# Performance work log

Hardware: AMD Instinct MI355X
Metric: run time of the kernel (lower is better)

## Reference

```python
import jax, jax.numpy as jnp
import numpy as np

N_NODES = 50000
N_EDGES = 800000
C = 128


def setup_inputs() -> dict:
    key = jax.random.key(0)
    ks = jax.random.split(key, 7)
    X_real = jax.random.normal(ks[0], (N_NODES, C), dtype=jnp.float32)
    X_imag = jax.random.normal(ks[1], (N_NODES, C), dtype=jnp.float32)
    # sparse normalized Laplacian values (real/imag parts), COO format
    L_real_vals = jax.random.normal(ks[2], (N_EDGES,), dtype=jnp.float32) * 0.1
    L_imag_vals = jax.random.normal(ks[3], (N_EDGES,), dtype=jnp.float32) * 0.1
    weight = jax.random.normal(ks[4], (C, C), dtype=jnp.float32) * (1.0 / np.sqrt(C))
    row = jax.random.randint(ks[5], (N_EDGES,), 0, N_NODES, dtype=jnp.int32)
    col = jax.random.randint(ks[6], (N_EDGES,), 0, N_NODES, dtype=jnp.int32)
    return {"X_real": X_real, "X_imag": X_imag,
            "L_real_vals": L_real_vals, "L_imag_vals": L_imag_vals,
            "weight": weight, "row": row, "col": col}


def reference(X_real, X_imag, L_real_vals, L_imag_vals, weight, row, col):
    n = X_real.shape[0]

    def spmm(vals, X):
        # sparse [N,N] @ dense [N,C] via gather + segment-sum scatter
        return jax.ops.segment_sum(vals[:, None] * X[col], row, num_segments=n)

    # complex Laplacian application: (Lr + i Li)(Xr + i Xi)
    # real = Lr@Xr - Li@Xi ; imag = Li@Xr + Lr@Xi ; then shared dense projection W
    agg_real = spmm(L_real_vals, X_real) - spmm(L_imag_vals, X_imag)  # [N, C]
    agg_imag = spmm(L_imag_vals, X_real) + spmm(L_real_vals, X_imag)  # [N, C]
    result_real = agg_real @ weight
    result_imag = agg_imag @ weight
    # residual add as in forward()
    return (result_real + X_real, result_imag + X_imag)
```

## Files before the change

kernel.cpp:

```cpp
#include <hip/hip_runtime.h>
#include <cstddef>

#define CC 128

typedef __attribute__((ext_vector_type(8))) short bf16x8;
typedef __attribute__((ext_vector_type(4))) float f32x4;


__device__ __forceinline__ unsigned short f2bf(float f)
{
    unsigned int u = __float_as_uint(f);
    u = (u + 0x7fffu + ((u >> 16) & 1u)) >> 16;
    return (unsigned short)u;
}

__device__ __forceinline__ unsigned int pack2(float a, float b)
{
    return (unsigned int)f2bf(a) | ((unsigned int)f2bf(b) << 16);
}

__global__ __launch_bounds__(256) void hist_conv_fused(
    const int* __restrict__ row, int* __restrict__ counts,
    int* __restrict__ rank, int N, int E,
    const float* __restrict__ W, unsigned short* __restrict__ Wt, int G_conv)
{
    const int bid = blockIdx.x;
    if (bid < G_conv) {
        const int idx = bid * 256 + threadIdx.x;
        if (idx >= CC * CC) return;
        const int k = idx >> 7;
        const int n = idx & 127;
        const unsigned int sw =
            ((unsigned)(2 * k) ^ (((unsigned)n & 7u) << 4)) >> 1;
        Wt[(size_t)n * 128 + sw] = f2bf(W[idx]);
        return;
    }
    const int base = ((bid - G_conv) * 256 + threadIdx.x) * 4;
    if (base + 3 < E) {
        const int4 r4 = *(const int4*)(row + base);
        int4 k4;
        k4.x = atomicAdd(counts + 0 * N + r4.x, 1);
        k4.y = atomicAdd(counts + 1 * N + r4.y, 1);
        k4.z = atomicAdd(counts + 2 * N + r4.z, 1);
        k4.w = atomicAdd(counts + 3 * N + r4.w, 1);
        *(int4*)(rank + base) = k4;
    } else {
        for (int e = base; e < E; ++e)
            rank[e] = atomicAdd(counts + (size_t)(e & 3) * N + row[e], 1);
    }
}

__global__ __launch_bounds__(256) void scan_block_reduce(
    const int* __restrict__ counts, int* __restrict__ bsum, int N)
{
    __shared__ int s[256];
    const int t = threadIdx.x;
    const int idx = blockIdx.x * 256 + t;
    int v = 0;
    if (idx < N)
        v = counts[idx] + counts[N + idx] + counts[2 * N + idx]
          + counts[3 * N + idx];
    s[t] = v;
    __syncthreads();
    #pragma unroll
    for (int off = 128; off > 0; off >>= 1) {
        if (t < off) s[t] += s[t + off];
        __syncthreads();
    }
    if (t == 0) bsum[blockIdx.x] = s[0];
}

__global__ __launch_bounds__(256) void scan_bsum(
    const int* __restrict__ bsum, int* __restrict__ bpre, int NB)
{
    __shared__ int s[256];
    const int t = threadIdx.x;
    s[t] = (t < NB) ? bsum[t] : 0;
    __syncthreads();
    #pragma unroll
    for (int off = 1; off < 256; off <<= 1) {
        const int v = s[t];
        const int u = (t >= off) ? s[t - off] : 0;
        __syncthreads();
        s[t] = v + u;
        __syncthreads();
    }
    if (t < NB) bpre[t] = t ? s[t - 1] : 0;
}

__global__ __launch_bounds__(256) void scan_final(
    const int* __restrict__ counts, const int* __restrict__ bpre,
    int* __restrict__ rbase, int N)
{
    __shared__ int s[256];
    const int t = threadIdx.x;
    const int idx = blockIdx.x * 256 + t;
    int c0 = 0, c1 = 0, c2 = 0, c3 = 0;
    if (idx < N) {
        c0 = counts[idx];
        c1 = counts[N + idx];
        c2 = counts[2 * N + idx];
        c3 = counts[3 * N + idx];
    }
    const int v = c0 + c1 + c2 + c3;
    s[t] = v;
    __syncthreads();
    #pragma unroll
    for (int off = 1; off < 256; off <<= 1) {
        const int a = s[t];
        const int u = (t >= off) ? s[t - off] : 0;
        __syncthreads();
        s[t] = a + u;
        __syncthreads();
    }
    if (idx < N) {
        const int off = bpre[blockIdx.x] + s[t] - v;
        rbase[idx]         = off;
        rbase[N + idx]     = off + c0;
        rbase[2 * N + idx] = off + c0 + c1;
        rbase[3 * N + idx] = off + c0 + c1 + c2;
    }
}

__device__ __forceinline__ void gemm_body(
    const float* __restrict__ Xr, const float* __restrict__ Xi,
    const unsigned short* __restrict__ Wt,
    unsigned short* __restrict__ Y, int N, int bid)
{
    __shared__ unsigned short Bs[128 * 128];
    __shared__ unsigned short As[64 * 128];
    const int t = threadIdx.x;
    const int m0 = bid * 64;
    const int M = 2 * N;

    {
        const uint4* src = (const uint4*)Wt;
        uint4* dst = (uint4*)Bs;
        #pragma unroll
        for (int i = 0; i < 8; ++i) dst[t + 256 * i] = src[t + 256 * i];
    }
    #pragma unroll
    for (int i = 0; i < 4; ++i) {
        const int blk = t + 256 * i;
        const int r  = blk >> 4;
        const int k0 = (blk & 15) * 8;
        const int m  = m0 + r;
        float4 q0 = make_float4(0.f, 0.f, 0.f, 0.f);
        float4 q1 = make_float4(0.f, 0.f, 0.f, 0.f);
        if (m < M) {
            const float* src = (m < N) ? (Xr + (size_t)m * CC)
                                       : (Xi + (size_t)(m - N) * CC);
            q0 = *(const float4*)(src + k0);
            q1 = *(const float4*)(src + k0 + 4);
        }
        uint4 h;
        h.x = pack2(q0.x, q0.y);
        h.y = pack2(q0.z, q0.w);
        h.z = pack2(q1.x, q1.y);
        h.w = pack2(q1.z, q1.w);
        const int byte = r * 256 + ((2 * k0) ^ ((r & 7) << 4));
        *(uint4*)((char*)As + byte) = h;
    }
    __syncthreads();

    const int w = t >> 6, lane = t & 63;
    const int wr = w >> 1, wc = w & 1;
    const int r0 = wr * 32;
    const int c0 = wc * 64;
    const int lr = lane & 15;
    const int lk = lane >> 4;

    f32x4 acc[2][4];
    #pragma unroll
    for (int a = 0; a < 2; ++a)
        #pragma unroll
        for (int b = 0; b < 4; ++b)
            acc[a][b] = (f32x4){0.f, 0.f, 0.f, 0.f};

    #pragma unroll
    for (int kk = 0; kk < 4; ++kk) {
        const int kbase = kk * 32 + lk * 8;
        bf16x8 afrag[2];
        #pragma unroll
        for (int at = 0; at < 2; ++at) {
            const int row = r0 + at * 16 + lr;
            afrag[at] = *(const bf16x8*)((const char*)As +
                row * 256 + ((2 * kbase) ^ ((row & 7) << 4)));
        }
        #pragma unroll
        for (int bt = 0; bt < 4; ++bt) {
            const int col = c0 + bt * 16 + lr;
            const bf16x8 bfrag = *(const bf16x8*)((const char*)Bs +
                col * 256 + ((2 * kbase) ^ ((col & 7) << 4)));
            acc[0][bt] = __builtin_amdgcn_mfma_f32_16x16x32_bf16(
                afrag[0], bfrag, acc[0][bt], 0, 0, 0);
            acc[1][bt] = __builtin_amdgcn_mfma_f32_16x16x32_bf16(
                afrag[1], bfrag, acc[1][bt], 0, 0, 0);
        }
    }

    #pragma unroll
    for (int at = 0; at < 2; ++at) {
        #pragma unroll
        for (int v = 0; v < 4; ++v) {
            const int m = m0 + r0 + at * 16 + lk * 4 + v;
            if (m >= M) continue;
            const int node = (m < N) ? m : m - N;
            const int half = (m < N) ? 0 : 128;
            unsigned short* dst = Y + (size_t)node * 256 + half;
            #pragma unroll
            for (int bt = 0; bt < 4; ++bt)
                dst[c0 + bt * 16 + lr] = f2bf(acc[at][bt][v]);
        }
    }
}

__device__ __forceinline__ void fill_body(
    const int* __restrict__ row, const int* __restrict__ col,
    const float* __restrict__ Lr, const float* __restrict__ Li,
    const int* __restrict__ rbase, const int* __restrict__ rank,
    int4* __restrict__ meta, int N, int E, int bid)
{
    const int base = (bid * 256 + threadIdx.x) * 4;
    if (base + 3 < E) {
        const int4   r4 = *(const int4*)(row + base);
        const int4   c4 = *(const int4*)(col + base);
        const float4 a4 = *(const float4*)(Lr + base);
        const float4 b4 = *(const float4*)(Li + base);
        const int4   k4 = *(const int4*)(rank + base);
        meta[rbase[r4.x] + k4.x] =
            make_int4(c4.x, __float_as_int(a4.x), __float_as_int(b4.x), 0);
        meta[rbase[N + r4.y] + k4.y] =
            make_int4(c4.y, __float_as_int(a4.y), __float_as_int(b4.y), 0);
        meta[rbase[2 * N + r4.z] + k4.z] =
            make_int4(c4.z, __float_as_int(a4.z), __float_as_int(b4.z), 0);
        meta[rbase[3 * N + r4.w] + k4.w] =
            make_int4(c4.w, __float_as_int(a4.w), __float_as_int(b4.w), 0);
    } else {
        for (int e = base; e < E; ++e)
            meta[rbase[(size_t)(e & 3) * N + row[e]] + rank[e]] =
                make_int4(col[e], __float_as_int(Lr[e]), __float_as_int(Li[e]), 0);
    }
}

__global__ __launch_bounds__(256) void fill_gemm_fused(
    const int* __restrict__ row, const int* __restrict__ col,
    const float* __restrict__ Lr, const float* __restrict__ Li,
    const int* __restrict__ rbase, const int* __restrict__ rank,
    int4* __restrict__ meta,
    const float* __restrict__ Xr, const float* __restrict__ Xi,
    const unsigned short* __restrict__ Wt, unsigned short* __restrict__ Y,
    int N, int E, int G_gemm)
{
    const int bid = blockIdx.x;
    if (bid < G_gemm)
        gemm_body(Xr, Xi, Wt, Y, N, bid);
    else
        fill_body(row, col, Lr, Li, rbase, rank, meta, N, E, bid - G_gemm);
}

__device__ __forceinline__ void cmadd_bf(
    const int4 m, const unsigned int ur, const unsigned int ui,
    float2& aR, float2& aI)
{
    const float lr = __int_as_float(m.y);
    const float li = __int_as_float(m.z);
    const float yrx = __uint_as_float(ur << 16);
    const float yry = __uint_as_float(ur & 0xFFFF0000u);
    const float yix = __uint_as_float(ui << 16);
    const float yiy = __uint_as_float(ui & 0xFFFF0000u);
    aR.x += lr * yrx - li * yix;
    aR.y += lr * yry - li * yiy;
    aI.x += li * yrx + lr * yix;
    aI.y += li * yry + lr * yiy;
}

__device__ __forceinline__ void edge_acc(
    const int4 m, const unsigned short* __restrict__ Y,
    int lane, float2& aR, float2& aI)
{
    const unsigned short* b = Y + (size_t)m.x * 256 + 2 * lane;
    const unsigned int ur = *(const unsigned int*)(b);
    const unsigned int ui = *(const unsigned int*)(b + 128);
    cmadd_bf(m, ur, ui, aR, aI);
}

__global__ __launch_bounds__(256) void gather_fused(
    const unsigned short* __restrict__ Y,
    const float* __restrict__ Xr, const float* __restrict__ Xi,
    const int* __restrict__ offsets, const int4* __restrict__ meta,
    float* __restrict__ out, int N, int E)
{
    const int n = blockIdx.x * 4 + (threadIdx.x >> 6);
    if (n >= N) return;
    const int lane = threadIdx.x & 63;
    const int start = offsets[n];
    const int end   = (n + 1 < N) ? offsets[n + 1] : E;
    const int Em1 = E - 1;

    float2 aR = *(const float2*)(Xr + (size_t)n * CC + 2 * lane);
    float2 aI = *(const float2*)(Xi + (size_t)n * CC + 2 * lane);

    int4 m0 = meta[min(start + 0, Em1)];
    int4 m1 = meta[min(start + 1, Em1)];
    int4 m2 = meta[min(start + 2, Em1)];
    int4 m3 = meta[min(start + 3, Em1)];
    int4 m4 = meta[min(start + 4, Em1)];
    int4 m5 = meta[min(start + 5, Em1)];
    int4 m6 = meta[min(start + 6, Em1)];
    int4 m7 = meta[min(start + 7, Em1)];

    int j = start;
    for (; j + 8 <= end; j += 8) {
        const int4 n0 = meta[min(j +  8, Em1)];
        const int4 n1 = meta[min(j +  9, Em1)];
        const int4 n2 = meta[min(j + 10, Em1)];
        const int4 n3 = meta[min(j + 11, Em1)];
        const int4 n4 = meta[min(j + 12, Em1)];
        const int4 n5 = meta[min(j + 13, Em1)];
        const int4 n6 = meta[min(j + 14, Em1)];
        const int4 n7 = meta[min(j + 15, Em1)];
        const unsigned short* b0 = Y + (size_t)m0.x * 256 + 2 * lane;
        const unsigned short* b1 = Y + (size_t)m1.x * 256 + 2 * lane;
        const unsigned short* b2 = Y + (size_t)m2.x * 256 + 2 * lane;
        const unsigned short* b3 = Y + (size_t)m3.x * 256 + 2 * lane;
        const unsigned short* b4 = Y + (size_t)m4.x * 256 + 2 * lane;
        const unsigned short* b5 = Y + (size_t)m5.x * 256 + 2 * lane;
        const unsigned short* b6 = Y + (size_t)m6.x * 256 + 2 * lane;
        const unsigned short* b7 = Y + (size_t)m7.x * 256 + 2 * lane;
        const unsigned int ur0 = *(const unsigned int*)(b0);
        const unsigned int ui0 = *(const unsigned int*)(b0 + 128);
        const unsigned int ur1 = *(const unsigned int*)(b1);
        const unsigned int ui1 = *(const unsigned int*)(b1 + 128);
        const unsigned int ur2 = *(const unsigned int*)(b2);
        const unsigned int ui2 = *(const unsigned int*)(b2 + 128);
        const unsigned int ur3 = *(const unsigned int*)(b3);
        const unsigned int ui3 = *(const unsigned int*)(b3 + 128);
        const unsigned int ur4 = *(const unsigned int*)(b4);
        const unsigned int ui4 = *(const unsigned int*)(b4 + 128);
        const unsigned int ur5 = *(const unsigned int*)(b5);
        const unsigned int ui5 = *(const unsigned int*)(b5 + 128);
        const unsigned int ur6 = *(const unsigned int*)(b6);
        const unsigned int ui6 = *(const unsigned int*)(b6 + 128);
        const unsigned int ur7 = *(const unsigned int*)(b7);
        const unsigned int ui7 = *(const unsigned int*)(b7 + 128);

        cmadd_bf(m0, ur0, ui0, aR, aI);
        cmadd_bf(m1, ur1, ui1, aR, aI);
        cmadd_bf(m2, ur2, ui2, aR, aI);
        cmadd_bf(m3, ur3, ui3, aR, aI);
        cmadd_bf(m4, ur4, ui4, aR, aI);
        cmadd_bf(m5, ur5, ui5, aR, aI);
        cmadd_bf(m6, ur6, ui6, aR, aI);
        cmadd_bf(m7, ur7, ui7, aR, aI);

        m0 = n0; m1 = n1; m2 = n2; m3 = n3;
        m4 = n4; m5 = n5; m6 = n6; m7 = n7;
    }
    const int r = end - j;
    if (r > 0) edge_acc(m0, Y, lane, aR, aI);
    if (r > 1) edge_acc(m1, Y, lane, aR, aI);
    if (r > 2) edge_acc(m2, Y, lane, aR, aI);
    if (r > 3) edge_acc(m3, Y, lane, aR, aI);
    if (r > 4) edge_acc(m4, Y, lane, aR, aI);
    if (r > 5) edge_acc(m5, Y, lane, aR, aI);
    if (r > 6) edge_acc(m6, Y, lane, aR, aI);

    *(float2*)(out + (size_t)n * CC + 2 * lane) = aR;
    *(float2*)(out + ((size_t)n + N) * CC + 2 * lane) = aI;
}

__global__ __launch_bounds__(256) void gather_nodes(
    const float* __restrict__ Xr, const float* __restrict__ Xi,
    const int* __restrict__ offsets, const int4* __restrict__ meta,
    float* __restrict__ out, int N, int E)
{
    const int n = blockIdx.x * 4 + (threadIdx.x >> 6);
    if (n >= N) return;
    const int lane = threadIdx.x & 63;
    const int start = offsets[n];
    const int end   = (n + 1 < N) ? offsets[n + 1] : E;
    float2 aR = make_float2(0.f, 0.f);
    float2 aI = make_float2(0.f, 0.f);
    for (int j = start; j < end; ++j) {
        const int4 m0 = meta[j];
        const float2 xr0 = *(const float2*)(Xr + (size_t)m0.x * CC + 2 * lane);
        const float2 xi0 = *(const float2*)(Xi + (size_t)m0.x * CC + 2 * lane);
        const float lr0 = __int_as_float(m0.y), li0 = __int_as_float(m0.z);
        aR.x += lr0 * xr0.x - li0 * xi0.x;
        aR.y += lr0 * xr0.y - li0 * xi0.y;
        aI.x += li0 * xr0.x + lr0 * xi0.x;
        aI.y += li0 * xr0.y + lr0 * xi0.y;
    }
    *(float2*)(out + (size_t)n * CC + 2 * lane) = aR;
    *(float2*)(out + ((size_t)n + N) * CC + 2 * lane) = aI;
}

__global__ __launch_bounds__(256) void scatter_edges(
    const float* __restrict__ Xr, const float* __restrict__ Xi,
    const float* __restrict__ Lr, const float* __restrict__ Li,
    const int* __restrict__ row, const int* __restrict__ col,
    float* __restrict__ out, int N, int E)
{
    const int e = blockIdx.x * 4 + (threadIdx.x >> 6);
    if (e >= E) return;
    const int lane = threadIdx.x & 63;
    const int r = row[e], c = col[e];
    const float lr = Lr[e];
    const float li = Li[e];
    const float2 xr = *(const float2*)(Xr + (size_t)c * CC + 2 * lane);
    const float2 xi = *(const float2*)(Xi + (size_t)c * CC + 2 * lane);
    float* pr = out + (size_t)r * CC + 2 * lane;
    float* pi = out + ((size_t)r + N) * CC + 2 * lane;
    unsafeAtomicAdd(pr,     lr * xr.x - li * xi.x);
    unsafeAtomicAdd(pr + 1, lr * xr.y - li * xi.y);
    unsafeAtomicAdd(pi,     li * xr.x + lr * xi.x);
    unsafeAtomicAdd(pi + 1, li * xr.y + lr * xi.y);
}

__global__ __launch_bounds__(256) void hist_rank_fb(
    const int* __restrict__ row, int* __restrict__ counts,
    int* __restrict__ rank, int N, int E)
{
    const int base = (blockIdx.x * 256 + threadIdx.x) * 4;
    if (base + 3 < E) {
        const int4 r4 = *(const int4*)(row + base);
        int4 k4;
        k4.x = atomicAdd(counts + 0 * N + r4.x, 1);
        k4.y = atomicAdd(counts + 1 * N + r4.y, 1);
        k4.z = atomicAdd(counts + 2 * N + r4.z, 1);
        k4.w = atomicAdd(counts + 3 * N + r4.w, 1);
        *(int4*)(rank + base) = k4;
    } else {
        for (int e = base; e < E; ++e)
            rank[e] = atomicAdd(counts + (size_t)(e & 3) * N + row[e], 1);
    }
}

__global__ __launch_bounds__(256) void fill_csr_fb(
    const int* __restrict__ row, const int* __restrict__ col,
    const float* __restrict__ Lr, const float* __restrict__ Li,
    const int* __restrict__ rbase, const int* __restrict__ rank,
    int4* __restrict__ meta, int N, int E)
{
    fill_body(row, col, Lr, Li, rbase, rank, meta, N, E, blockIdx.x);
}

__global__ __launch_bounds__(256) void gemm_inplace(
    float* __restrict__ io, const float* __restrict__ W,
    const float* __restrict__ Xp, int N)
{
    __shared__ float Ws[64 * CC];
    __shared__ float AsT[CC][36];
    const int t = threadIdx.x;
    const int m0 = blockIdx.x * 32;

    for (int ch = t; ch < 1024; ch += 256) {
        const int r  = ch >> 5;
        const int k0 = (ch & 31) * 4;
        const int m  = m0 + r;
        float4 q = make_float4(0.f, 0.f, 0.f, 0.f);
        if (m < N) q = *(const float4*)(io + (size_t)m * CC + k0);
        AsT[k0 + 0][r] = q.x;
        AsT[k0 + 1][r] = q.y;
        AsT[k0 + 2][r] = q.z;
        AsT[k0 + 3][r] = q.w;
    }

    const int cg = t & 31;
    const int rs = t >> 5;
    float s[4][4];
    #pragma unroll
    for (int a = 0; a < 4; ++a)
        #pragma unroll
        for (int b = 0; b < 4; ++b) s[a][b] = 0.f;

    for (int kc = 0; kc < 2; ++kc) {
        __syncthreads();
        {
            const float4* src = (const float4*)(W + (size_t)kc * 64 * CC);
            float4* dst = (float4*)Ws;
            #pragma unroll
            for (int i = 0; i < 8; ++i) dst[t + 256 * i] = src[t + 256 * i];
        }
        __syncthreads();
        #pragma unroll 4
        for (int kk = 0; kk < 64; ++kk) {
            const int k = kc * 64 + kk;
            const float4 av = *(const float4*)&AsT[k][rs * 4];
            const float4 wv = *(const float4*)&Ws[kk * CC + cg * 4];
            const float ar[4] = {av.x, av.y, av.z, av.w};
            const float wc[4] = {wv.x, wv.y, wv.z, wv.w};
            #pragma unroll
            for (int a = 0; a < 4; ++a)
                #pragma unroll
                for (int b = 0; b < 4; ++b) s[a][b] += ar[a] * wc[b];
        }
    }

    #pragma unroll
    for (int a = 0; a < 4; ++a) {
        const int m = m0 + rs * 4 + a;
        if (m >= N) continue;
        const float4 xv = *(const float4*)(Xp + (size_t)m * CC + cg * 4);
        float4 o;
        o.x = s[a][0] + xv.x;
        o.y = s[a][1] + xv.y;
        o.z = s[a][2] + xv.z;
        o.w = s[a][3] + xv.w;
        *(float4*)(io + (size_t)m * CC + cg * 4) = o;
    }
}

extern "C" void kernel_launch(void* const* d_in, const int* in_sizes, int n_in,
                              void* d_out, int out_size, void* d_ws, size_t ws_size,
                              hipStream_t stream)
{
    const float* Xr = (const float*)d_in[0];
    const float* Xi = (const float*)d_in[1];
    const float* Lr = (const float*)d_in[2];
    const float* Li = (const float*)d_in[3];
    const float* W  = (const float*)d_in[4];
    const int* row = (const int*)d_in[5];
    const int* col = (const int*)d_in[6];
    float* out = (float*)d_out;

    const int N = in_sizes[0] / CC;
    const int E = in_sizes[2];
    const int NB = (N + 255) / 256;
    const int EB4 = ((E + 3) / 4 + 255) / 256;
    const int G_conv = (CC * CC + 255) / 256;
    const int G_gemm = (2 * N + 63) / 64;

    const size_t y_bytes    = (size_t)N * 256 * sizeof(unsigned short);
    const size_t wt_bytes   = (size_t)CC * CC * sizeof(unsigned short);
    const size_t meta_bytes = (size_t)E * 16;
    const size_t int_bytes  = ((size_t)8 * N + 512 + E) * sizeof(int);
    const size_t need_csr   = meta_bytes + int_bytes;
    const size_t need_fused = y_bytes + wt_bytes + need_csr;

    if (ws_size >= need_fused) {
        unsigned short* Y  = (unsigned short*)d_ws;
        unsigned short* Wt = (unsigned short*)((char*)d_ws + y_bytes);
        int4*  meta   = (int4*)((char*)d_ws + y_bytes + wt_bytes);
        int*   counts = (int*)((char*)d_ws + y_bytes + wt_bytes + meta_bytes);
        int*   rbase  = counts + 4 * N;
        int*   bsum   = rbase + 4 * N;
        int*   bpre   = bsum + 256;
        int*   rank   = bpre + 256;

        hipMemsetAsync(counts, 0, (size_t)4 * N * sizeof(int), stream);
        hist_conv_fused<<<dim3(G_conv + EB4), dim3(256), 0, stream>>>(
            row, counts, rank, N, E, W, Wt, G_conv);
        scan_block_reduce<<<dim3(NB), dim3(256), 0, stream>>>(counts, bsum, N);
        scan_bsum<<<dim3(1), dim3(256), 0, stream>>>(bsum, bpre, NB);
        scan_final<<<dim3(NB), dim3(256), 0, stream>>>(counts, bpre, rbase, N);
        fill_gemm_fused<<<dim3(G_gemm + EB4), dim3(256), 0, stream>>>(
            row, col, Lr, Li, rbase, rank, meta, Xr, Xi, Wt, Y, N, E, G_gemm);
        gather_fused<<<dim3((N + 3) / 4), dim3(256), 0, stream>>>(
            Y, Xr, Xi, rbase , meta, out, N, E);
    } else if (ws_size >= need_csr) {
        int4* meta    = (int4*)d_ws;
        int*  counts  = (int*)((char*)d_ws + meta_bytes);
        int*  rbase   = counts + 4 * N;
        int*  bsum    = rbase + 4 * N;
        int*  bpre    = bsum + 256;
        int*  rank    = bpre + 256;

        hipMemsetAsync(counts, 0, (size_t)4 * N * sizeof(int), stream);
        hist_rank_fb<<<dim3(EB4), dim3(256), 0, stream>>>(row, counts, rank, N, E);
        scan_block_reduce<<<dim3(NB), dim3(256), 0, stream>>>(counts, bsum, N);
        scan_bsum<<<dim3(1), dim3(256), 0, stream>>>(bsum, bpre, NB);
        scan_final<<<dim3(NB), dim3(256), 0, stream>>>(counts, bpre, rbase, N);
        fill_csr_fb<<<dim3(EB4), dim3(256), 0, stream>>>(
            row, col, Lr, Li, rbase, rank, meta, N, E);
        gather_nodes<<<dim3((N + 3) / 4), dim3(256), 0, stream>>>(
            Xr, Xi, rbase, meta, out, N, E);
        gemm_inplace<<<dim3((N + 31) / 32), dim3(256), 0, stream>>>(out, W, Xr, N);
        gemm_inplace<<<dim3((N + 31) / 32), dim3(256), 0, stream>>>(
            out + (size_t)N * CC, W, Xi, N);
    } else {
        hipMemsetAsync(out, 0, (size_t)2 * N * CC * sizeof(float), stream);
        scatter_edges<<<dim3((E + 3) / 4), dim3(256), 0, stream>>>(
            Xr, Xi, Lr, Li, row, col, out, N, E);
        gemm_inplace<<<dim3((N + 31) / 32), dim3(256), 0, stream>>>(out, W, Xr, N);
        gemm_inplace<<<dim3((N + 31) / 32), dim3(256), 0, stream>>>(
            out + (size_t)N * CC, W, Xi, N);
    }
}
```

Measured before the change: 247.0 us.

## Fuse whole pipeline into one persistent cooperative kernel with grid syncs

Replaces the memset plus six separate launches (histogram, three scan stages, fill+GEMM, gather) with a single cooperative persistent kernel that loops over work and separates phases with grid-wide syncs. It also reorders work so the GEMM tile runs alongside the histogram phase, and loads the weight tile into LDS once per block instead of once per tile. The aim is to remove launch gaps and tail effects between many small kernels. The trade-offs are the cost of grid syncs, a grid capped at occupancy-limited residency (48KB LDS per block), and persistent loops that may underuse the GPU in the gather phase. If the cooperative launch fails, it falls back to the old multi-kernel path.

```diff
diff --git a/kernel.cpp b/kernel.cpp
--- a/kernel.cpp
+++ b/kernel.cpp
@@ -1,11 +1,13 @@
 #include <hip/hip_runtime.h>
+#include <hip/hip_cooperative_groups.h>
 #include <cstddef>
 
 #define CC 128
+
+namespace cg = cooperative_groups;
 
 typedef __attribute__((ext_vector_type(8))) short bf16x8;
 typedef __attribute__((ext_vector_type(4))) float f32x4;
-
 
 __device__ __forceinline__ unsigned short f2bf(float f)
 {
@@ -19,126 +21,24 @@
     return (unsigned int)f2bf(a) | ((unsigned int)f2bf(b) << 16);
 }
 
-__global__ __launch_bounds__(256) void hist_conv_fused(
-    const int* __restrict__ row, int* __restrict__ counts,
-    int* __restrict__ rank, int N, int E,
-    const float* __restrict__ W, unsigned short* __restrict__ Wt, int G_conv)
-{
-    const int bid = blockIdx.x;
-    if (bid < G_conv) {
-        const int idx = bid * 256 + threadIdx.x;
-        if (idx >= CC * CC) return;
-        const int k = idx >> 7;
-        const int n = idx & 127;
-        const unsigned int sw =
-            ((unsigned)(2 * k) ^ (((unsigned)n & 7u) << 4)) >> 1;
-        Wt[(size_t)n * 128 + sw] = f2bf(W[idx]);
-        return;
-    }
-    const int base = ((bid - G_conv) * 256 + threadIdx.x) * 4;
-    if (base + 3 < E) {
-        const int4 r4 = *(const int4*)(row + base);
-        int4 k4;
-        k4.x = atomicAdd(counts + 0 * N + r4.x, 1);
-        k4.y = atomicAdd(counts + 1 * N + r4.y, 1);
-        k4.z = atomicAdd(counts + 2 * N + r4.z, 1);
-        k4.w = atomicAdd(counts + 3 * N + r4.w, 1);
-        *(int4*)(rank + base) = k4;
-    } else {
-        for (int e = base; e < E; ++e)
-            rank[e] = atomicAdd(counts + (size_t)(e & 3) * N + row[e], 1);
-    }
-}
-
-__global__ __launch_bounds__(256) void scan_block_reduce(
-    const int* __restrict__ counts, int* __restrict__ bsum, int N)
-{
-    __shared__ int s[256];
-    const int t = threadIdx.x;
-    const int idx = blockIdx.x * 256 + t;
-    int v = 0;
-    if (idx < N)
-        v = counts[idx] + counts[N + idx] + counts[2 * N + idx]
-          + counts[3 * N + idx];
-    s[t] = v;
-    __syncthreads();
-    #pragma unroll
-    for (int off = 128; off > 0; off >>= 1) {
-        if (t < off) s[t] += s[t + off];
-        __syncthreads();
-    }
-    if (t == 0) bsum[blockIdx.x] = s[0];
-}
-
-__global__ __launch_bounds__(256) void scan_bsum(
-    const int* __restrict__ bsum, int* __restrict__ bpre, int NB)
-{
-    __shared__ int s[256];
-    const int t = threadIdx.x;
-    s[t] = (t < NB) ? bsum[t] : 0;
-    __syncthreads();
-    #pragma unroll
-    for (int off = 1; off < 256; off <<= 1) {
-        const int v = s[t];
-        const int u = (t >= off) ? s[t - off] : 0;
-        __syncthreads();
-        s[t] = v + u;
-        __syncthreads();
-    }
-    if (t < NB) bpre[t] = t ? s[t - 1] : 0;
-}
-
-__global__ __launch_bounds__(256) void scan_final(
-    const int* __restrict__ counts, const int* __restrict__ bpre,
-    int* __restrict__ rbase, int N)
-{
-    __shared__ int s[256];
-    const int t = threadIdx.x;
-    const int idx = blockIdx.x * 256 + t;
-    int c0 = 0, c1 = 0, c2 = 0, c3 = 0;
-    if (idx < N) {
-        c0 = counts[idx];
-        c1 = counts[N + idx];
-        c2 = counts[2 * N + idx];
-        c3 = counts[3 * N + idx];
-    }
-    const int v = c0 + c1 + c2 + c3;
-    s[t] = v;
-    __syncthreads();
-    #pragma unroll
-    for (int off = 1; off < 256; off <<= 1) {
-        const int a = s[t];
-        const int u = (t >= off) ? s[t - off] : 0;
-        __syncthreads();
-        s[t] = a + u;
-        __syncthreads();
-    }
-    if (idx < N) {
-        const int off = bpre[blockIdx.x] + s[t] - v;
-        rbase[idx]         = off;
-        rbase[N + idx]     = off + c0;
-        rbase[2 * N + idx] = off + c0 + c1;
-        rbase[3 * N + idx] = off + c0 + c1 + c2;
-    }
-}
-
-__device__ __forceinline__ void gemm_body(
+
+__device__ __forceinline__ void gemm_stage_B(
+    const unsigned short* __restrict__ Wt, unsigned short* Bs, int t)
+{
+    const uint4* src = (const uint4*)Wt;
+    uint4* dst = (uint4*)Bs;
+    #pragma unroll
+    for (int i = 0; i < 8; ++i) dst[t + 256 * i] = src[t + 256 * i];
+}
+
+__device__ __forceinline__ void gemm_tile(
     const float* __restrict__ Xr, const float* __restrict__ Xi,
-    const unsigned short* __restrict__ Wt,
-    unsigned short* __restrict__ Y, int N, int bid)
-{
-    __shared__ unsigned short Bs[128 * 128];
-    __shared__ unsigned short As[64 * 128];
-    const int t = threadIdx.x;
+    unsigned short* __restrict__ Y, int N, int bid,
+    const unsigned short* Bs, unsigned short* As, int t)
+{
     const int m0 = bid * 64;
     const int M = 2 * N;
 
-    {
-        const uint4* src = (const uint4*)Wt;
-        uint4* dst = (uint4*)Bs;
-        #pragma unroll
-        for (int i = 0; i < 8; ++i) dst[t + 256 * i] = src[t + 256 * i];
-    }
     #pragma unroll
     for (int i = 0; i < 4; ++i) {
         const int blk = t + 256 * i;
@@ -215,13 +115,12 @@
     }
 }
 
-__device__ __forceinline__ void fill_body(
+__device__ __forceinline__ void fill_quad(
     const int* __restrict__ row, const int* __restrict__ col,
     const float* __restrict__ Lr, const float* __restrict__ Li,
     const int* __restrict__ rbase, const int* __restrict__ rank,
-    int4* __restrict__ meta, int N, int E, int bid)
-{
-    const int base = (bid * 256 + threadIdx.x) * 4;
+    int4* __restrict__ meta, int N, int E, int base)
+{
     if (base + 3 < E) {
         const int4   r4 = *(const int4*)(row + base);
         const int4   c4 = *(const int4*)(col + base);
@@ -243,20 +142,22 @@
     }
 }
 
-__global__ __launch_bounds__(256) void fill_gemm_fused(
-    const int* __restrict__ row, const int* __restrict__ col,
-    const float* __restrict__ Lr, const float* __restrict__ Li,
-    const int* __restrict__ rbase, const int* __restrict__ rank,
-    int4* __restrict__ meta,
-    const float* __restrict__ Xr, const float* __restrict__ Xi,
-    const unsigned short* __restrict__ Wt, unsigned short* __restrict__ Y,
-    int N, int E, int G_gemm)
-{
-    const int bid = blockIdx.x;
-    if (bid < G_gemm)
-        gemm_body(Xr, Xi, Wt, Y, N, bid);
-    else
-        fill_body(row, col, Lr, Li, rbase, rank, meta, N, E, bid - G_gemm);
+__device__ __forceinline__ void hist_quad(
+    const int* __restrict__ row, int* __restrict__ counts,
+    int* __restrict__ rank, int N, int E, int base)
+{
+    if (base + 3 < E) {
+        const int4 r4 = *(const int4*)(row + base);
+        int4 k4;
+        k4.x = atomicAdd(counts + 0 * N + r4.x, 1);
+        k4.y = atomicAdd(counts + 1 * N + r4.y, 1);
+        k4.z = atomicAdd(counts + 2 * N + r4.z, 1);
+        k4.w = atomicAdd(counts + 3 * N + r4.w, 1);
+        *(int4*)(rank + base) = k4;
+    } else {
+        for (int e = base; e < E; ++e)
+            rank[e] = atomicAdd(counts + (size_t)(e & 3) * N + row[e], 1);
+    }
 }
 
 __device__ __forceinline__ void cmadd_bf(
@@ -285,15 +186,12 @@
     cmadd_bf(m, ur, ui, aR, aI);
 }
 
-__global__ __launch_bounds__(256) void gather_fused(
+__device__ __forceinline__ void gather_node(
     const unsigned short* __restrict__ Y,
     const float* __restrict__ Xr, const float* __restrict__ Xi,
     const int* __restrict__ offsets, const int4* __restrict__ meta,
-    float* __restrict__ out, int N, int E)
-{
-    const int n = blockIdx.x * 4 + (threadIdx.x >> 6);
-    if (n >= N) return;
-    const int lane = threadIdx.x & 63;
+    float* __restrict__ out, int N, int E, int n, int lane)
+{
     const int start = offsets[n];
     const int end   = (n + 1 < N) ? offsets[n + 1] : E;
     const int Em1 = E - 1;
@@ -370,6 +268,254 @@
     *(float2*)(out + ((size_t)n + N) * CC + 2 * lane) = aI;
 }
 
+__global__ __launch_bounds__(256) void mega(
+    const int* __restrict__ row, const int* __restrict__ col,
+    const float* __restrict__ Lr, const float* __restrict__ Li,
+    const float* __restrict__ W,
+    const float* __restrict__ Xr, const float* __restrict__ Xi,
+    int* __restrict__ counts, int* __restrict__ rank,
+    int* __restrict__ rbase, int* __restrict__ bsum, int* __restrict__ bpre,
+    int4* __restrict__ meta, unsigned short* __restrict__ Wt,
+    unsigned short* __restrict__ Y, float* __restrict__ out,
+    int N, int E, int NB, int G_gemm)
+{
+    cg::grid_group gg = cg::this_grid();
+    __shared__ char smem[49152];
+    unsigned short* Bs = (unsigned short*)smem;
+    unsigned short* As = (unsigned short*)(smem + 32768);
+    int* si = (int*)smem;
+
+    const int t  = threadIdx.x;
+    const int gb = blockIdx.x;
+    const int G  = gridDim.x;
+    const int NQ = (E + 3) >> 2;
+
+    for (int i = gb * 256 + t; i < 4 * N; i += G * 256) counts[i] = 0;
+    for (int idx = gb * 256 + t; idx < CC * CC; idx += G * 256) {
+        const int k = idx >> 7;
+        const int n = idx & 127;
+        const unsigned int sw =
+            ((unsigned)(2 * k) ^ (((unsigned)n & 7u) << 4)) >> 1;
+        Wt[(size_t)n * 128 + sw] = f2bf(W[idx]);
+    }
+    gg.sync();
+
+    gemm_stage_B(Wt, Bs, t);
+    for (int bid = gb; bid < G_gemm; bid += G) {
+        __syncthreads();
+        gemm_tile(Xr, Xi, Y, N, bid, Bs, As, t);
+    }
+    for (int qi = gb * 256 + t; qi < NQ; qi += G * 256)
+        hist_quad(row, counts, rank, N, E, qi * 4);
+    gg.sync();
+
+    for (int b = gb; b < NB; b += G) {
+        const int idx = b * 256 + t;
+        int v = 0;
+        if (idx < N)
+            v = counts[idx] + counts[N + idx] + counts[2 * N + idx]
+              + counts[3 * N + idx];
+        si[t] = v;
+        __syncthreads();
+        #pragma unroll
+        for (int off = 128; off > 0; off >>= 1) {
+            if (t < off) si[t] += si[t + off];
+            __syncthreads();
+        }
+        if (t == 0) bsum[b] = si[0];
+        __syncthreads();
+    }
+    gg.sync();
+
+    if (gb == 0) {
+        si[t] = (t < NB) ? bsum[t] : 0;
+        __syncthreads();
+        #pragma unroll
+        for (int off = 1; off < 256; off <<= 1) {
+            const int v = si[t];
+            const int u = (t >= off) ? si[t - off] : 0;
+            __syncthreads();
+            si[t] = v + u;
+            __syncthreads();
+        }
+        if (t < NB) bpre[t] = t ? si[t - 1] : 0;
+    }
+    gg.sync();
+
+    for (int b = gb; b < NB; b += G) {
+        const int idx = b * 256 + t;
+        int c0 = 0, c1 = 0, c2 = 0, c3 = 0;
+        if (idx < N) {
+            c0 = counts[idx];
+            c1 = counts[N + idx];
+            c2 = counts[2 * N + idx];
+            c3 = counts[3 * N + idx];
+        }
+        const int v = c0 + c1 + c2 + c3;
+        si[t] = v;
+        __syncthreads();
+        #pragma unroll
+        for (int off = 1; off < 256; off <<= 1) {
+            const int a = si[t];
+            const int u = (t >= off) ? si[t - off] : 0;
+            __syncthreads();
+            si[t] = a + u;
+            __syncthreads();
+        }
+        if (idx < N) {
+            const int off = bpre[b] + si[t] - v;
+            rbase[idx]         = off;
+            rbase[N + idx]     = off + c0;
+            rbase[2 * N + idx] = off + c0 + c1;
+            rbase[3 * N + idx] = off + c0 + c1 + c2;
+        }
+        __syncthreads();
+    }
+    gg.sync();
+
+    for (int qi = gb * 256 + t; qi < NQ; qi += G * 256)
+        fill_quad(row, col, Lr, Li, rbase, rank, meta, N, E, qi * 4);
+    gg.sync();
+
+    {
+        const int lane = t & 63;
+        const int wv = t >> 6;
+        const int NG = (N + 3) / 4;
+        for (int g = gb; g < NG; g += G) {
+            const int n = g * 4 + wv;
+            if (n < N)
+                gather_node(Y, Xr, Xi, rbase , meta, out, N, E,
+                            n, lane);
+        }
+    }
+}
+
+
+__global__ __launch_bounds__(256) void hist_conv_fused(
+    const int* __restrict__ row, int* __restrict__ counts,
+    int* __restrict__ rank, int N, int E,
+    const float* __restrict__ W, unsigned short* __restrict__ Wt, int G_conv)
+{
+    const int bid = blockIdx.x;
+    if (bid < G_conv) {
+        const int idx = bid * 256 + threadIdx.x;
+        if (idx >= CC * CC) return;
+        const int k = idx >> 7;
+        const int n = idx & 127;
+        const unsigned int sw =
+            ((unsigned)(2 * k) ^ (((unsigned)n & 7u) << 4)) >> 1;
+        Wt[(size_t)n * 128 + sw] = f2bf(W[idx]);
+        return;
+    }
+    hist_quad(row, counts, rank, N, E,
+              ((bid - G_conv) * 256 + threadIdx.x) * 4);
+}
+
+__global__ __launch_bounds__(256) void scan_block_reduce(
+    const int* __restrict__ counts, int* __restrict__ bsum, int N)
+{
+    __shared__ int s[256];
+    const int t = threadIdx.x;
+    const int idx = blockIdx.x * 256 + t;
+    int v = 0;
+    if (idx < N)
+        v = counts[idx] + counts[N + idx] + counts[2 * N + idx]
+          + counts[3 * N + idx];
+    s[t] = v;
+    __syncthreads();
+    #pragma unroll
+    for (int off = 128; off > 0; off >>= 1) {
+        if (t < off) s[t] += s[t + off];
+        __syncthreads();
+    }
+    if (t == 0) bsum[blockIdx.x] = s[0];
+}
+
+__global__ __launch_bounds__(256) void scan_bsum(
+    const int* __restrict__ bsum, int* __restrict__ bpre, int NB)
+{
+    __shared__ int s[256];
+    const int t = threadIdx.x;
+    s[t] = (t < NB) ? bsum[t] : 0;
+    __syncthreads();
+    #pragma unroll
+    for (int off = 1; off < 256; off <<= 1) {
+        const int v = s[t];
+        const int u = (t >= off) ? s[t - off] : 0;
+        __syncthreads();
+        s[t] = v + u;
+        __syncthreads();
+    }
+    if (t < NB) bpre[t] = t ? s[t - 1] : 0;
+}
+
+__global__ __launch_bounds__(256) void scan_final(
+    const int* __restrict__ counts, const int* __restrict__ bpre,
+    int* __restrict__ rbase, int N)
+{
+    __shared__ int s[256];
+    const int t = threadIdx.x;
+    const int idx = blockIdx.x * 256 + t;
+    int c0 = 0, c1 = 0, c2 = 0, c3 = 0;
+    if (idx < N) {
+        c0 = counts[idx];
+        c1 = counts[N + idx];
+        c2 = counts[2 * N + idx];
+        c3 = counts[3 * N + idx];
+    }
+    const int v = c0 + c1 + c2 + c3;
+    s[t] = v;
+    __syncthreads();
+    #pragma unroll
+    for (int off = 1; off < 256; off <<= 1) {
+        const int a = s[t];
+        const int u = (t >= off) ? s[t - off] : 0;
+        __syncthreads();
+        s[t] = a + u;
+        __syncthreads();
+    }
+    if (idx < N) {
+        const int off = bpre[blockIdx.x] + s[t] - v;
+        rbase[idx]         = off;
+        rbase[N + idx]     = off + c0;
+        rbase[2 * N + idx] = off + c0 + c1;
+        rbase[3 * N + idx] = off + c0 + c1 + c2;
+    }
+}
+
+__global__ __launch_bounds__(256) void fill_gemm_fused(
+    const int* __restrict__ row, const int* __restrict__ col,
+    const float* __restrict__ Lr, const float* __restrict__ Li,
+    const int* __restrict__ rbase, const int* __restrict__ rank,
+    int4* __restrict__ meta,
+    const float* __restrict__ Xr, const float* __restrict__ Xi,
+    const unsigned short* __restrict__ Wt, unsigned short* __restrict__ Y,
+    int N, int E, int G_gemm)
+{
+    __shared__ char smem[49152];
+    const int bid = blockIdx.x;
+    if (bid < G_gemm) {
+        unsigned short* Bs = (unsigned short*)smem;
+        unsigned short* As = (unsigned short*)(smem + 32768);
+        gemm_stage_B(Wt, Bs, threadIdx.x);
+        gemm_tile(Xr, Xi, Y, N, bid, Bs, As, threadIdx.x);
+    } else {
+        fill_quad(row, col, Lr, Li, rbase, rank, meta, N, E,
+                  ((bid - G_gemm) * 256 + threadIdx.x) * 4);
+    }
+}
+
+__global__ __launch_bounds__(256) void gather_fused(
+    const unsigned short* __restrict__ Y,
+    const float* __restrict__ Xr, const float* __restrict__ Xi,
+    const int* __restrict__ offsets, const int4* __restrict__ meta,
+    float* __restrict__ out, int N, int E)
+{
+    const int n = blockIdx.x * 4 + (threadIdx.x >> 6);
+    if (n >= N) return;
+    gather_node(Y, Xr, Xi, offsets, meta, out, N, E, n, threadIdx.x & 63);
+}
+
 __global__ __launch_bounds__(256) void gather_nodes(
     const float* __restrict__ Xr, const float* __restrict__ Xi,
     const int* __restrict__ offsets, const int4* __restrict__ meta,
@@ -422,19 +568,8 @@
     const int* __restrict__ row, int* __restrict__ counts,
     int* __restrict__ rank, int N, int E)
 {
-    const int base = (blockIdx.x * 256 + threadIdx.x) * 4;
-    if (base + 3 < E) {
-        const int4 r4 = *(const int4*)(row + base);
-        int4 k4;
-        k4.x = atomicAdd(counts + 0 * N + r4.x, 1);
-        k4.y = atomicAdd(counts + 1 * N + r4.y, 1);
-        k4.z = atomicAdd(counts + 2 * N + r4.z, 1);
-        k4.w = atomicAdd(counts + 3 * N + r4.w, 1);
-        *(int4*)(rank + base) = k4;
-    } else {
-        for (int e = base; e < E; ++e)
-            rank[e] = atomicAdd(counts + (size_t)(e & 3) * N + row[e], 1);
-    }
+    hist_quad(row, counts, rank, N, E,
+              (blockIdx.x * 256 + threadIdx.x) * 4);
 }
 
 __global__ __launch_bounds__(256) void fill_csr_fb(
@@ -443,7 +578,8 @@
     const int* __restrict__ rbase, const int* __restrict__ rank,
     int4* __restrict__ meta, int N, int E)
 {
-    fill_body(row, col, Lr, Li, rbase, rank, meta, N, E, blockIdx.x);
+    fill_quad(row, col, Lr, Li, rbase, rank, meta, N, E,
+              (blockIdx.x * 256 + threadIdx.x) * 4);
 }
 
 __global__ __launch_bounds__(256) void gemm_inplace(
@@ -467,7 +603,7 @@
         AsT[k0 + 3][r] = q.w;
     }
 
-    const int cg = t & 31;
+    const int cg_ = t & 31;
     const int rs = t >> 5;
     float s[4][4];
     #pragma unroll
@@ -488,7 +624,7 @@
         for (int kk = 0; kk < 64; ++kk) {
             const int k = kc * 64 + kk;
             const float4 av = *(const float4*)&AsT[k][rs * 4];
-            const float4 wv = *(const float4*)&Ws[kk * CC + cg * 4];
+            const float4 wv = *(const float4*)&Ws[kk * CC + cg_ * 4];
             const float ar[4] = {av.x, av.y, av.z, av.w};
             const float wc[4] = {wv.x, wv.y, wv.z, wv.w};
             #pragma unroll
@@ -502,13 +638,13 @@
     for (int a = 0; a < 4; ++a) {
         const int m = m0 + rs * 4 + a;
         if (m >= N) continue;
-        const float4 xv = *(const float4*)(Xp + (size_t)m * CC + cg * 4);
+        const float4 xv = *(const float4*)(Xp + (size_t)m * CC + cg_ * 4);
         float4 o;
         o.x = s[a][0] + xv.x;
         o.y = s[a][1] + xv.y;
         o.z = s[a][2] + xv.z;
         o.w = s[a][3] + xv.w;
-        *(float4*)(io + (size_t)m * CC + cg * 4) = o;
+        *(float4*)(io + (size_t)m * CC + cg_ * 4) = o;
     }
 }
 
@@ -525,12 +661,12 @@
     const int* col = (const int*)d_in[6];
     float* out = (float*)d_out;
 
-    const int N = in_sizes[0] / CC;
-    const int E = in_sizes[2];
-    const int NB = (N + 255) / 256;
+    int N = in_sizes[0] / CC;
+    int E = in_sizes[2];
+    int NB = (N + 255) / 256;
     const int EB4 = ((E + 3) / 4 + 255) / 256;
     const int G_conv = (CC * CC + 255) / 256;
-    const int G_gemm = (2 * N + 63) / 64;
+    int G_gemm = (2 * N + 63) / 64;
 
     const size_t y_bytes    = (size_t)N * 256 * sizeof(unsigned short);
     const size_t wt_bytes   = (size_t)CC * CC * sizeof(unsigned short);
@@ -538,6 +674,23 @@
     const size_t int_bytes  = ((size_t)8 * N + 512 + E) * sizeof(int);
     const size_t need_csr   = meta_bytes + int_bytes;
     const size_t need_fused = y_bytes + wt_bytes + need_csr;
+
+    static int mega_grid = -2;
+    if (mega_grid == -2) {
+        mega_grid = 0;
+        int dev = 0, coop = 0, ncu = 0, bpc = 0;
+        if (hipGetDevice(&dev) == hipSuccess &&
+            hipDeviceGetAttribute(&coop, hipDeviceAttributeCooperativeLaunch,
+                                  dev) == hipSuccess && coop &&
+            hipDeviceGetAttribute(&ncu,
+                                  hipDeviceAttributeMultiprocessorCount,
+                                  dev) == hipSuccess && ncu > 0 &&
+            hipOccupancyMaxActiveBlocksPerMultiprocessor(
+                &bpc, reinterpret_cast<const void*>(mega), 256, 0)
+                == hipSuccess && bpc > 0) {
+            mega_grid = bpc * ncu;
+        }
+    }
 
     if (ws_size >= need_fused) {
         unsigned short* Y  = (unsigned short*)d_ws;
@@ -549,16 +702,32 @@
         int*   bpre   = bsum + 256;
         int*   rank   = bpre + 256;
 
-        hipMemsetAsync(counts, 0, (size_t)4 * N * sizeof(int), stream);
-        hist_conv_fused<<<dim3(G_conv + EB4), dim3(256), 0, stream>>>(
-            row, counts, rank, N, E, W, Wt, G_conv);
-        scan_block_reduce<<<dim3(NB), dim3(256), 0, stream>>>(counts, bsum, N);
-        scan_bsum<<<dim3(1), dim3(256), 0, stream>>>(bsum, bpre, NB);
-        scan_final<<<dim3(NB), dim3(256), 0, stream>>>(counts, bpre, rbase, N);
-        fill_gemm_fused<<<dim3(G_gemm + EB4), dim3(256), 0, stream>>>(
-            row, col, Lr, Li, rbase, rank, meta, Xr, Xi, Wt, Y, N, E, G_gemm);
-        gather_fused<<<dim3((N + 3) / 4), dim3(256), 0, stream>>>(
-            Y, Xr, Xi, rbase , meta, out, N, E);
+        bool launched = false;
+        if (mega_grid > 0) {
+            void* kargs[] = {
+                (void*)&row, (void*)&col, (void*)&Lr, (void*)&Li,
+                (void*)&W, (void*)&Xr, (void*)&Xi,
+                (void*)&counts, (void*)&rank, (void*)&rbase,
+                (void*)&bsum, (void*)&bpre,
+                (void*)&meta, (void*)&Wt, (void*)&Y, (void*)&out,
+                (void*)&N, (void*)&E, (void*)&NB, (void*)&G_gemm };
+            launched = hipLaunchCooperativeKernel(
+                reinterpret_cast<const void*>(mega),
+                dim3(mega_grid), dim3(256), kargs, 0, stream) == hipSuccess;
+            if (!launched) mega_grid = 0;
+        }
+        if (!launched) {
+            hipMemsetAsync(counts, 0, (size_t)4 * N * sizeof(int), stream);
+            hist_conv_fused<<<dim3(G_conv + EB4), dim3(256), 0, stream>>>(
+                row, counts, rank, N, E, W, Wt, G_conv);
+            scan_block_reduce<<<dim3(NB), dim3(256), 0, stream>>>(counts, bsum, N);
+            scan_bsum<<<dim3(1), dim3(256), 0, stream>>>(bsum, bpre, NB);
+            scan_final<<<dim3(NB), dim3(256), 0, stream>>>(counts, bpre, rbase, N);
+            fill_gemm_fused<<<dim3(G_gemm + EB4), dim3(256), 0, stream>>>(
+                row, col, Lr, Li, rbase, rank, meta, Xr, Xi, Wt, Y, N, E, G_gemm);
+            gather_fused<<<dim3((N + 3) / 4), dim3(256), 0, stream>>>(
+                Y, Xr, Xi, rbase, meta, out, N, E);
+        }
     } else if (ws_size >= need_csr) {
         int4* meta    = (int4*)d_ws;
         int*  counts  = (int*)((char*)d_ws + meta_bytes);
```

Result: slower. 537.6 us (+117.7%).
